# Performance work log

Measured on AMD Instinct MI355X. Metric: run time of the kernel, lower is better.

Reference implementation:

```python
import jax, jax.numpy as jnp
import numpy as np

N_EXPR, MAX_TOK, D = 8192, 32, 256
N_SYM, N_APP = 50000, 262144


def gate(prev, upd, Wg, bg, Wc, bc):
    # NDFA-style gated update: f*prev + (1-f)*candidate
    cat = jnp.concatenate([prev, upd], axis=-1)            # [N, 2D]
    f = jax.nn.sigmoid(cat @ Wg + bg)                      # [N, D]
    cand = jax.nn.relu(cat @ Wc + bc)                      # [N, D]
    return f * prev + (1.0 - f) * cand


def setup_inputs() -> dict:
    key = jax.random.key(0)
    ks = jax.random.split(key, 12)
    s = 1.0 / np.sqrt(2 * D)
    return {
        "expressions_encodings": jax.random.normal(ks[0], (N_EXPR, MAX_TOK, D), jnp.float32),
        "symbols_encodings": jax.random.normal(ks[1], (N_SYM, D), jnp.float32),
        "prev_cfg_nodes_encodings": jax.random.normal(ks[2], (N_EXPR, D), jnp.float32),
        "Wg1": jax.random.normal(ks[3], (2 * D, D), jnp.float32) * s,
        "bg1": jnp.zeros((D,), jnp.float32),
        "Wc1": jax.random.normal(ks[4], (2 * D, D), jnp.float32) * s,
        "bc1": jnp.zeros((D,), jnp.float32),
        "Wg2": jax.random.normal(ks[5], (2 * D, D), jnp.float32) * s,
        "bg2": jnp.zeros((D,), jnp.float32),
        "Wc2": jax.random.normal(ks[6], (2 * D, D), jnp.float32) * s,
        "bc2": jnp.zeros((D,), jnp.float32),
        "app_expr_idx": jax.random.randint(ks[7], (N_APP,), 0, N_EXPR, jnp.int32),
        "app_token_idx": jax.random.randint(ks[8], (N_APP,), 0, MAX_TOK, jnp.int32),
        "app_symbol_idx": jax.random.randint(ks[9], (N_APP,), 0, N_SYM, jnp.int32),
        "cfg_nodes_has_expression_mask": jnp.ones((N_EXPR,), jnp.bool_),
    }


def reference(expressions_encodings, symbols_encodings, prev_cfg_nodes_encodings,
              Wg1, bg1, Wc1, bc1, Wg2, bg2, Wc2, bc2,
              app_expr_idx, app_token_idx, app_symbol_idx,
              cfg_nodes_has_expression_mask):
    # --- AddSymbolsEncodingsToExpressions: gather -> gate -> scatter ---
    flat_idx = app_expr_idx * MAX_TOK + app_token_idx      # [N_APP]
    flat = expressions_encodings.reshape(-1, D)            # [N_EXPR*MAX_TOK, D]
    symbols_occurrences = flat[flat_idx]                   # gather [N_APP, D]
    sym_enc_for_occ = symbols_encodings[app_symbol_idx]    # gather [N_APP, D]
    updated_occ = gate(symbols_occurrences, sym_enc_for_occ, Wg1, bg1, Wc1, bc1)
    flat = flat.at[flat_idx].set(updated_occ)              # scatter (last-write like torch.scatter)
    updated_expressions = flat.reshape(N_EXPR, MAX_TOK, D)

    # --- combine tokens per expression (combiner proxy: mean over tokens) ---
    cfg_combined_expressions = updated_expressions.mean(axis=1)   # [N_EXPR, D]

    # --- CFGNodeEncodingMixerWithExpressionEncoding: gate + masked scatter ---
    gated_nodes = gate(prev_cfg_nodes_encodings, cfg_combined_expressions, Wg2, bg2, Wc2, bc2)
    new_nodes = jnp.where(cfg_nodes_has_expression_mask[:, None], gated_nodes,
                          prev_cfg_nodes_encodings)
    return new_nodes
```

## Files before the change

kernel.cpp:

```cpp
#include <hip/hip_runtime.h>
#include <hip/hip_bf16.h>

typedef __attribute__((ext_vector_type(8))) short bf16x8;
typedef __attribute__((ext_vector_type(4))) float f32x4;

#define NE 8192
#define MT 32
#define DD 256
#define NAPP 262144
#define NSLOT (NE*MT)
#define NSYM 50000
#define NSYMP 50048

#define WS_WINNER 0
#define WS_WTSW   (1u<<20)
#define WS_WTLIN  (2u<<20)
#define WS_SYMGC  (3u<<20)

static __device__ __forceinline__ unsigned short f2b(float x){
  union{float f; unsigned u;} v; v.f = x;
  unsigned r = (v.u + 0x7fffu + ((v.u>>16)&1u))>>16;
  return (unsigned short)r;
}
static __device__ __forceinline__ unsigned pk2(float a, float b){
  return (unsigned)f2b(a) | ((unsigned)f2b(b)<<16);
}
static __device__ __forceinline__ float bfl(unsigned w){ union{unsigned u; float f;} v; v.u = w<<16; return v.f; }
static __device__ __forceinline__ float bfh(unsigned w){ union{unsigned u; float f;} v; v.u = w & 0xffff0000u; return v.f; }
static __device__ __forceinline__ float frombf(unsigned short u){ union{unsigned x; float f;} v; v.x = ((unsigned)u)<<16; return v.f; }

static __device__ __forceinline__ void gload16(const void* g, void* l){
  __builtin_amdgcn_global_load_lds((const __attribute__((address_space(1))) void*)g,
                                   (__attribute__((address_space(3))) void*)l, 16, 0, 0);
}

__global__ void k_wt(const float* __restrict__ w0, const float* __restrict__ w1,
                     const float* __restrict__ w2, const float* __restrict__ w3,
                     char* __restrict__ wtsw, unsigned short* __restrict__ wtlin){
  int g = blockIdx.x*256 + threadIdx.x;
  int m = g >> 14;
  int kg = (g >> 8) & 63;
  int n = g & 255;
  const float* W = (m==0)?w0:(m==1)?w1:(m==2)?w2:w3;
  unsigned short v[8];
  #pragma unroll
  for (int i=0;i<8;i++) v[i] = f2b(W[(kg*8+i)*DD + n]);
  uint4 u;
  u.x = (unsigned)v[0] | ((unsigned)v[1]<<16);
  u.y = (unsigned)v[2] | ((unsigned)v[3]<<16);
  u.z = (unsigned)v[4] | ((unsigned)v[5]<<16);
  u.w = (unsigned)v[6] | ((unsigned)v[7]<<16);
  *(uint4*)(wtlin + (size_t)m*131072 + n*512 + kg*8) = u;
  int rot = ((kg & 3) + (n >> 1)) & 3;
  *(uint4*)(wtsw + (size_t)m*262144 + n*1024 + (kg>>2)*64 + rot*16) = u;
}

__global__ void k_winner(const int* __restrict__ ei, const int* __restrict__ ti,
                         int* __restrict__ winner){
  int i = blockIdx.x*256 + threadIdx.x;
  atomicMax(&winner[ei[i]*MT + ti[i]], i);
}

__global__ __launch_bounds__(512, 4)
void k_syms(const float* __restrict__ sym, const char* __restrict__ wtsw,
            unsigned short* __restrict__ symgc){
  __shared__ char Abuf[32768];
  __shared__ char Bbuf[32768];

  int tid = threadIdx.x, lane = tid & 63, wv = tid >> 6;
  int l15 = lane & 15, lg = lane >> 4;
  int wq = wv & 3; bool isC = wv >= 4;
  int s0 = blockIdx.x * 64;

  {
    int r = tid >> 3;
    int row = s0 + r;
    char* arow = Abuf + r*512;
    unsigned swz = (unsigned)((r & 15) << 4);
    if (row < NSYM){
      const float* src = sym + (size_t)row*DD;
      #pragma unroll
      for (int i=0;i<4;i++){
        int c = (tid & 7) + i*8;
        float4 x = *(const float4*)(src + c*8);
        float4 y = *(const float4*)(src + c*8 + 4);
        uint4 u; u.x=pk2(x.x,x.y); u.y=pk2(x.z,x.w); u.z=pk2(y.x,y.y); u.w=pk2(y.z,y.w);
        *(uint4*)(arow + ((c*16) ^ swz)) = u;
      }
    } else {
      uint4 u = {0,0,0,0};
      #pragma unroll
      for (int i=0;i<4;i++){
        int c = (tid & 7) + i*8;
        *(uint4*)(arow + ((c*16) ^ swz)) = u;
      }
    }
  }
  __syncthreads();

  f32x4 acc[4][4];
  f32x4 zz = {0.f,0.f,0.f,0.f};
  #pragma unroll
  for (int rt=0;rt<4;rt++)
    #pragma unroll
    for (int ct=0;ct<4;ct++) acc[rt][ct]=zz;

  const char* wbG = wtsw;
  const char* wbC = wtsw + 262144;

  for (int kt=0; kt<8; ++kt){
    __syncthreads();
    #pragma unroll
    for (int i=0;i<4;i++){
      int n = wv*64 + i*16 + (lane>>2);
      const char* src = ((n < 256)? wbG : wbC) + (size_t)(n & 255)*1024 + (8+kt)*64 + (lane&3)*16;
      gload16(src, Bbuf + n*64 + (lane&3)*16);
    }
    __syncthreads();
    int koff = kt*64 + lg*16;
    bf16x8 a[4], b[4];
    #pragma unroll
    for (int rt=0;rt<4;rt++)
      a[rt] = *(const bf16x8*)(Abuf + (rt*16 + l15)*512 + (koff ^ (l15<<4)));
    #pragma unroll
    for (int ct=0;ct<4;ct++){
      int nn = (isC?256:0) + wq*64 + ct*16 + l15;
      b[ct] = *(const bf16x8*)(Bbuf + nn*64 + (((lg + (nn>>1)) & 3)<<4));
    }
    #pragma unroll
    for (int rt=0;rt<4;rt++)
      #pragma unroll
      for (int ct=0;ct<4;ct++)
        acc[rt][ct] = __builtin_amdgcn_mfma_f32_16x16x32_bf16(a[rt], b[ct], acc[rt][ct], 0,0,0);
  }

  int cb = (isC?256:0) + wq*64;
  #pragma unroll
  for (int rt=0;rt<4;rt++)
    #pragma unroll
    for (int ct=0;ct<4;ct++)
      #pragma unroll
      for (int j=0;j<4;j++){
        int row = s0 + rt*16 + lg*4 + j;
        symgc[(size_t)row*512 + cb + ct*16 + l15] = f2b(acc[rt][ct][j]);
      }
}

__global__ __launch_bounds__(512, 4)
void k_gate1(const float* __restrict__ expr, const char* __restrict__ wtsw,
             const float* __restrict__ bg, const float* __restrict__ bc,
             const int* __restrict__ winner, const int* __restrict__ appsym,
             const unsigned short* __restrict__ symgc,
             float* __restrict__ outcomb){
  __shared__ char Abuf[32768];
  __shared__ char Bbuf[32768];

  int tid = threadIdx.x, lane = tid & 63, wv = tid >> 6;
  int l15 = lane & 15, lg = lane >> 4;
  int wq = wv & 3; bool isC = wv >= 4;
  int s0 = blockIdx.x * 64;

  int wn = winner[s0 + lane];
  int sidv = (wn >= 0) ? appsym[wn] : -1;

  {
    int r = tid >> 3;
    const float* src = expr + (size_t)(s0 + r)*DD;
    char* arow = Abuf + r*512;
    unsigned swz = (unsigned)((r & 15) << 4);
    #pragma unroll
    for (int i=0;i<4;i++){
      int c = (tid & 7) + i*8;
      float4 x = *(const float4*)(src + c*8);
      float4 y = *(const float4*)(src + c*8 + 4);
      uint4 u; u.x=pk2(x.x,x.y); u.y=pk2(x.z,x.w); u.z=pk2(y.x,y.y); u.w=pk2(y.z,y.w);
      *(uint4*)(arow + ((c*16) ^ swz)) = u;
    }
  }
  __syncthreads();

  f32x4 acc[4][4];
  f32x4 zz = {0.f,0.f,0.f,0.f};
  #pragma unroll
  for (int rt=0;rt<4;rt++)
    #pragma unroll
    for (int ct=0;ct<4;ct++) acc[rt][ct]=zz;

  const char* wbG = wtsw;
  const char* wbC = wtsw + 262144;

  for (int kt=0; kt<8; ++kt){
    __syncthreads();
    #pragma unroll
    for (int i=0;i<4;i++){
      int n = wv*64 + i*16 + (lane>>2);
      const char* src = ((n < 256)? wbG : wbC) + (size_t)(n & 255)*1024 + kt*64 + (lane&3)*16;
      gload16(src, Bbuf + n*64 + (lane&3)*16);
    }
    __syncthreads();
    int koff = kt*64 + lg*16;
    bf16x8 a[4], b[4];
    #pragma unroll
    for (int rt=0;rt<4;rt++)
      a[rt] = *(const bf16x8*)(Abuf + (rt*16 + l15)*512 + (koff ^ (l15<<4)));
    #pragma unroll
    for (int ct=0;ct<4;ct++){
      int nn = (isC?256:0) + wq*64 + ct*16 + l15;
      b[ct] = *(const bf16x8*)(Bbuf + nn*64 + (((lg + (nn>>1)) & 3)<<4));
    }
    #pragma unroll
    for (int rt=0;rt<4;rt++)
      #pragma unroll
      for (int ct=0;ct<4;ct++)
        acc[rt][ct] = __builtin_amdgcn_mfma_f32_16x16x32_bf16(a[rt], b[ct], acc[rt][ct], 0,0,0);
  }

  __syncthreads();
  char* fbuf = Abuf;
  char* cbuf = Bbuf;
  char* obuf = isC ? cbuf : fbuf;

  const float* bias = isC ? bc : bg;
  float bv[4];
  #pragma unroll
  for (int ct=0;ct<4;ct++) bv[ct] = bias[wq*64 + ct*16 + l15];

  #pragma unroll
  for (int rt=0;rt<4;rt++){
    int rowb = rt*16 + lg*4;
    int sid[4];
    #pragma unroll
    for (int j=0;j<4;j++){ int s = __shfl(sidv, rowb + j); sid[j] = (s < 0) ? 0 : s; }
    float sv[4][4];
    #pragma unroll
    for (int j=0;j<4;j++)
      #pragma unroll
      for (int ct=0;ct<4;ct++)
        sv[j][ct] = frombf(symgc[(size_t)sid[j]*512 + (isC?256:0) + wq*64 + ct*16 + l15]);
    #pragma unroll
    for (int ct=0;ct<4;ct++){
      float o[4];
      #pragma unroll
      for (int j=0;j<4;j++){
        float x = acc[rt][ct][j] + sv[j][ct] + bv[ct];
        o[j] = isC ? fmaxf(x, 0.f) : 1.f/(1.f + __expf(-x));
      }
      int col = wq*64 + ct*16 + l15;
      uint2 pw; pw.x = pk2(o[0], o[1]); pw.y = pk2(o[2], o[3]);
      *(uint2*)(obuf + ((col*128 + rowb*2) ^ ((col&15)<<3))) = pw;
    }
  }
  __syncthreads();

  {
    int eL = wv >> 2, q = wv & 3;
    int col = q*64 + lane;
    float ssum = 0.f;
    #pragma unroll
    for (int i=0;i<8;i++){
      unsigned xr = (unsigned)((col*128 + eL*64 + i*8) ^ ((col&15)<<3));
      uint2 fu = *(const uint2*)(fbuf + xr);
      uint2 cu = *(const uint2*)(cbuf + xr);
      float fvv[4] = { bfl(fu.x), bfh(fu.x), bfl(fu.y), bfh(fu.y) };
      float cvv[4] = { bfl(cu.x), bfh(cu.x), bfl(cu.y), bfh(cu.y) };
      #pragma unroll
      for (int j=0;j<4;j++){
        int row = eL*32 + i*4 + j;
        float pv = expr[(size_t)(s0 + row)*DD + col];
        int sact = __shfl(sidv, row);
        ssum += (sact >= 0) ? (fvv[j]*pv + (1.f - fvv[j])*cvv[j]) : pv;
      }
    }
    outcomb[(size_t)(blockIdx.x*2 + eL)*DD + col] = ssum * (1.f/32.f);
  }
}

__global__ __launch_bounds__(1024)
void k_gate2(const float* __restrict__ prevn, const float* comb,
             const float* __restrict__ bg, const float* __restrict__ bc,
             const unsigned short* __restrict__ Wgt, const unsigned short* __restrict__ Wct,
             float* out){
  __shared__ char A[64*1024];

  int tid  = threadIdx.x;
  int lane = tid & 63;
  int wv   = tid >> 6;
  int wr = wv >> 3, wc = wv & 7;
  int l15 = lane & 15, lg = lane >> 4;
  int e0 = blockIdx.x * 64;

  {
    int row = tid >> 4, cb = (tid & 15)*16;
    unsigned swz = (unsigned)((row&7)<<4);
    const float* src = prevn + (size_t)(e0+row)*DD + cb;
    const float* s2  = comb  + (size_t)(e0+row)*DD + cb;
    char* arow = A + row*1024;
    #pragma unroll
    for (int i=0;i<2;i++){
      float4 x = *(const float4*)(src + i*8);
      float4 y = *(const float4*)(src + i*8 + 4);
      uint4 u; u.x=pk2(x.x,x.y); u.y=pk2(x.z,x.w); u.z=pk2(y.x,y.y); u.w=pk2(y.z,y.w);
      *(uint4*)(arow + (((cb+i*8)*2) ^ swz)) = u;
    }
    #pragma unroll
    for (int i=0;i<2;i++){
      float4 x = *(const float4*)(s2 + i*8);
      float4 y = *(const float4*)(s2 + i*8 + 4);
      uint4 u; u.x=pk2(x.x,x.y); u.y=pk2(x.z,x.w); u.z=pk2(y.x,y.y); u.w=pk2(y.z,y.w);
      *(uint4*)(arow + (((256+cb+i*8)*2) ^ swz)) = u;
    }
  }
  __syncthreads();

  unsigned swzL = (unsigned)((l15&7)<<4);
  const char* pa0 = A + (wr*32 + l15)*1024;
  const char* pa1 = pa0 + 16*1024;
  const unsigned short* wg0 = Wgt + (size_t)(wc*32 + l15)*512 + lg*8;
  const unsigned short* wc0 = Wct + (size_t)(wc*32 + l15)*512 + lg*8;

  f32x4 accg[2][2], accc[2][2];
  f32x4 zz = {0.f,0.f,0.f,0.f};
  #pragma unroll
  for (int ri=0;ri<2;ri++){ accg[ri][0]=zz; accg[ri][1]=zz; accc[ri][0]=zz; accc[ri][1]=zz; }

  for (int ks=0; ks<16; ++ks){
    int koff = (ks*64 + lg*16) ^ (int)swzL;
    bf16x8 a0 = *(const bf16x8*)(pa0 + koff);
    bf16x8 a1 = *(const bf16x8*)(pa1 + koff);
    int kw = ks*32;
    #pragma unroll
    for (int ct=0; ct<2; ++ct){
      bf16x8 b = *(const bf16x8*)(wg0 + ct*16*512 + kw);
      accg[0][ct] = __builtin_amdgcn_mfma_f32_16x16x32_bf16(a0, b, accg[0][ct], 0,0,0);
      accg[1][ct] = __builtin_amdgcn_mfma_f32_16x16x32_bf16(a1, b, accg[1][ct], 0,0,0);
    }
  }

  float bgv[2], bcv[2];
  #pragma unroll
  for (int ct=0;ct<2;ct++){ int c = wc*32+ct*16+l15; bgv[ct]=bg[c]; bcv[ct]=bc[c]; }
  #pragma unroll
  for (int ri=0;ri<2;ri++)
    #pragma unroll
    for (int ct=0;ct<2;ct++)
      #pragma unroll
      for (int j=0;j<4;j++)
        accg[ri][ct][j] = 1.f/(1.f + __expf(-(accg[ri][ct][j] + bgv[ct])));

  for (int ks=0; ks<16; ++ks){
    int koff = (ks*64 + lg*16) ^ (int)swzL;
    bf16x8 a0 = *(const bf16x8*)(pa0 + koff);
    bf16x8 a1 = *(const bf16x8*)(pa1 + koff);
    int kw = ks*32;
    #pragma unroll
    for (int ct=0; ct<2; ++ct){
      bf16x8 b = *(const bf16x8*)(wc0 + ct*16*512 + kw);
      accc[0][ct] = __builtin_amdgcn_mfma_f32_16x16x32_bf16(a0, b, accc[0][ct], 0,0,0);
      accc[1][ct] = __builtin_amdgcn_mfma_f32_16x16x32_bf16(a1, b, accc[1][ct], 0,0,0);
    }
  }

  #pragma unroll
  for (int ct=0; ct<2; ++ct){
    #pragma unroll
    for (int ri=0; ri<2; ++ri){
      #pragma unroll
      for (int j=0;j<4;j++){
        int row = wr*32 + ri*16 + lg*4 + j;
        int col = wc*32 + ct*16 + l15;
        int e = e0 + row;
        float prevv = prevn[(size_t)e*DD + col];
        float fr = accg[ri][ct][j];
        float cand = fmaxf(accc[ri][ct][j] + bcv[ct], 0.f);
        out[(size_t)e*DD + col] = fr*prevv + (1.f-fr)*cand;
      }
    }
  }
}

extern "C" void kernel_launch(void* const* d_in, const int* in_sizes, int n_in,
                              void* d_out, int out_size, void* d_ws, size_t ws_size,
                              hipStream_t stream){
  const float* expr = (const float*)d_in[0];
  const float* sym  = (const float*)d_in[1];
  const float* prevn= (const float*)d_in[2];
  const float* Wg1 = (const float*)d_in[3];
  const float* bg1 = (const float*)d_in[4];
  const float* Wc1 = (const float*)d_in[5];
  const float* bc1 = (const float*)d_in[6];
  const float* Wg2 = (const float*)d_in[7];
  const float* bg2 = (const float*)d_in[8];
  const float* Wc2 = (const float*)d_in[9];
  const float* bc2 = (const float*)d_in[10];
  const int* aei = (const int*)d_in[11];
  const int* ati = (const int*)d_in[12];
  const int* asi = (const int*)d_in[13];
  float* outp = (float*)d_out;

  char* wsb = (char*)d_ws;
  int* winner = (int*)(wsb + WS_WINNER);
  char* wtsw = wsb + WS_WTSW;
  unsigned short* wtlin = (unsigned short*)(wsb + WS_WTLIN);
  unsigned short* symgc = (unsigned short*)(wsb + WS_SYMGC);

  hipMemsetAsync(winner, 0xFF, NSLOT*sizeof(int), stream);
  k_wt<<<256, 256, 0, stream>>>(Wg1, Wc1, Wg2, Wc2, wtsw, wtlin);
  k_winner<<<NAPP/256, 256, 0, stream>>>(aei, ati, winner);
  k_syms<<<NSYMP/64, 512, 0, stream>>>(sym, wtsw, symgc);
  k_gate1<<<NSLOT/64, 512, 0, stream>>>(expr, wtsw, bg1, bc1, winner, asi, symgc, outp);
  k_gate2<<<NE/64, 1024, 0, stream>>>(prevn, outp, bg2, bc2,
                                      wtlin + 262144, wtlin + 393216, outp);
}
```

Baseline: 278.3 us.

## Restructure gate1 so each wave computes gate and candidate columns with register epilogue

Each wave now owns 32 output columns for both the gate and candidate GEMMs, so the sigmoid/relu combine and the token-mean reduction run directly in registers through shuffles. This removes the bf16 round-trip through LDS and the extra barriers. The symbol projection table is re-laid out so gate and candidate values for a lane sit together and load as one ushort4. Weight staging is split into separate G and C buffers whose loads are interleaved with the MFMAs. Launch bounds drop to 2 blocks per CU to leave room for the larger per-thread accumulator sets, at some risk to occupancy.

```diff
diff --git a/kernel.cpp b/kernel.cpp
--- a/kernel.cpp
+++ b/kernel.cpp
@@ -25,8 +25,6 @@
 static __device__ __forceinline__ unsigned pk2(float a, float b){
   return (unsigned)f2b(a) | ((unsigned)f2b(b)<<16);
 }
-static __device__ __forceinline__ float bfl(unsigned w){ union{unsigned u; float f;} v; v.u = w<<16; return v.f; }
-static __device__ __forceinline__ float bfh(unsigned w){ union{unsigned u; float f;} v; v.u = w & 0xffff0000u; return v.f; }
 static __device__ __forceinline__ float frombf(unsigned short u){ union{unsigned x; float f;} v; v.x = ((unsigned)u)<<16; return v.f; }
 
 static __device__ __forceinline__ void gload16(const void* g, void* l){
@@ -134,7 +132,6 @@
         acc[rt][ct] = __builtin_amdgcn_mfma_f32_16x16x32_bf16(a[rt], b[ct], acc[rt][ct], 0,0,0);
   }
 
-  int cb = (isC?256:0) + wq*64;
   #pragma unroll
   for (int rt=0;rt<4;rt++)
     #pragma unroll
@@ -142,31 +139,36 @@
       #pragma unroll
       for (int j=0;j<4;j++){
         int row = s0 + rt*16 + lg*4 + j;
-        symgc[(size_t)row*512 + cb + ct*16 + l15] = f2b(acc[rt][ct][j]);
-      }
-}
-
-__global__ __launch_bounds__(512, 4)
+        int idx = (wq*2 + (ct>>1))*64 + l15*4 + (ct&1)*2 + (isC?1:0);
+        symgc[(size_t)row*512 + idx] = f2b(acc[rt][ct][j]);
+      }
+}
+
+__global__ __launch_bounds__(512, 2)
 void k_gate1(const float* __restrict__ expr, const char* __restrict__ wtsw,
              const float* __restrict__ bg, const float* __restrict__ bc,
              const int* __restrict__ winner, const int* __restrict__ appsym,
              const unsigned short* __restrict__ symgc,
              float* __restrict__ outcomb){
-  __shared__ char Abuf[32768];
-  __shared__ char Bbuf[32768];
+  __shared__ char A[32768];
+  __shared__ char BGb[16384];
+  __shared__ char BCb[16384];
 
   int tid = threadIdx.x, lane = tid & 63, wv = tid >> 6;
   int l15 = lane & 15, lg = lane >> 4;
-  int wq = wv & 3; bool isC = wv >= 4;
   int s0 = blockIdx.x * 64;
 
   int wn = winner[s0 + lane];
-  int sidv = (wn >= 0) ? appsym[wn] : -1;
+  int sidv = (wn >= 0) ? appsym[wn] : 0;
+  unsigned long long hwmask = __ballot(wn >= 0);
+
+  const char* wsG = wtsw;
+  const char* wsC = wtsw + 262144;
 
   {
     int r = tid >> 3;
     const float* src = expr + (size_t)(s0 + r)*DD;
-    char* arow = Abuf + r*512;
+    char* arow = A + r*512;
     unsigned swz = (unsigned)((r & 15) << 4);
     #pragma unroll
     for (int i=0;i<4;i++){
@@ -177,102 +179,108 @@
       *(uint4*)(arow + ((c*16) ^ swz)) = u;
     }
   }
+  {
+    #pragma unroll
+    for (int i=0;i<2;i++){
+      int g = tid + i*512;
+      int n = g >> 2, p = g & 3;
+      gload16(wsG + (size_t)n*1024 + p*16, BGb + g*16);
+      gload16(wsC + (size_t)n*1024 + p*16, BCb + g*16);
+    }
+  }
   __syncthreads();
 
-  f32x4 acc[4][4];
+  f32x4 accG[4][2], accC[4][2];
   f32x4 zz = {0.f,0.f,0.f,0.f};
   #pragma unroll
-  for (int rt=0;rt<4;rt++)
-    #pragma unroll
-    for (int ct=0;ct<4;ct++) acc[rt][ct]=zz;
-
-  const char* wbG = wtsw;
-  const char* wbC = wtsw + 262144;
+  for (int rt=0;rt<4;rt++){ accG[rt][0]=zz; accG[rt][1]=zz; accC[rt][0]=zz; accC[rt][1]=zz; }
+
+  int nl0 = wv*32 + l15;
+  int rot0 = ((lg + (nl0>>1)) & 3) << 4;
+  int rot1 = ((lg + ((nl0+16)>>1)) & 3) << 4;
+  int boff0 = nl0*64 + rot0;
+  int boff1 = (nl0+16)*64 + rot1;
 
   for (int kt=0; kt<8; ++kt){
+    if (kt > 0){
+      #pragma unroll
+      for (int i=0;i<2;i++){
+        int g = tid + i*512;
+        int n = g >> 2, p = g & 3;
+        gload16(wsC + (size_t)n*1024 + kt*64 + p*16, BCb + g*16);
+      }
+    }
+    int koff = kt*64 + lg*16;
+    bf16x8 a[4];
+    #pragma unroll
+    for (int rt=0;rt<4;rt++)
+      a[rt] = *(const bf16x8*)(A + (rt*16 + l15)*512 + (koff ^ (l15<<4)));
+    {
+      bf16x8 b0 = *(const bf16x8*)(BGb + boff0);
+      bf16x8 b1 = *(const bf16x8*)(BGb + boff1);
+      #pragma unroll
+      for (int rt=0;rt<4;rt++){
+        accG[rt][0] = __builtin_amdgcn_mfma_f32_16x16x32_bf16(a[rt], b0, accG[rt][0], 0,0,0);
+        accG[rt][1] = __builtin_amdgcn_mfma_f32_16x16x32_bf16(a[rt], b1, accG[rt][1], 0,0,0);
+      }
+    }
     __syncthreads();
-    #pragma unroll
-    for (int i=0;i<4;i++){
-      int n = wv*64 + i*16 + (lane>>2);
-      const char* src = ((n < 256)? wbG : wbC) + (size_t)(n & 255)*1024 + kt*64 + (lane&3)*16;
-      gload16(src, Bbuf + n*64 + (lane&3)*16);
+    if (kt < 7){
+      #pragma unroll
+      for (int i=0;i<2;i++){
+        int g = tid + i*512;
+        int n = g >> 2, p = g & 3;
+        gload16(wsG + (size_t)n*1024 + (kt+1)*64 + p*16, BGb + g*16);
+      }
+    }
+    {
+      bf16x8 b0 = *(const bf16x8*)(BCb + boff0);
+      bf16x8 b1 = *(const bf16x8*)(BCb + boff1);
+      #pragma unroll
+      for (int rt=0;rt<4;rt++){
+        accC[rt][0] = __builtin_amdgcn_mfma_f32_16x16x32_bf16(a[rt], b0, accC[rt][0], 0,0,0);
+        accC[rt][1] = __builtin_amdgcn_mfma_f32_16x16x32_bf16(a[rt], b1, accC[rt][1], 0,0,0);
+      }
     }
     __syncthreads();
-    int koff = kt*64 + lg*16;
-    bf16x8 a[4], b[4];
-    #pragma unroll
-    for (int rt=0;rt<4;rt++)
-      a[rt] = *(const bf16x8*)(Abuf + (rt*16 + l15)*512 + (koff ^ (l15<<4)));
-    #pragma unroll
-    for (int ct=0;ct<4;ct++){
-      int nn = (isC?256:0) + wq*64 + ct*16 + l15;
-      b[ct] = *(const bf16x8*)(Bbuf + nn*64 + (((lg + (nn>>1)) & 3)<<4));
-    }
-    #pragma unroll
-    for (int rt=0;rt<4;rt++)
-      #pragma unroll
-      for (int ct=0;ct<4;ct++)
-        acc[rt][ct] = __builtin_amdgcn_mfma_f32_16x16x32_bf16(a[rt], b[ct], acc[rt][ct], 0,0,0);
-  }
-
-  __syncthreads();
-  char* fbuf = Abuf;
-  char* cbuf = Bbuf;
-  char* obuf = isC ? cbuf : fbuf;
-
-  const float* bias = isC ? bc : bg;
-  float bv[4];
-  #pragma unroll
-  for (int ct=0;ct<4;ct++) bv[ct] = bias[wq*64 + ct*16 + l15];
-
+  }
+
+  float bgv[2], bcv[2];
+  #pragma unroll
+  for (int ct=0;ct<2;ct++){ int c = wv*32+ct*16+l15; bgv[ct]=bg[c]; bcv[ct]=bc[c]; }
+
+  float osum[2][2] = {{0.f,0.f},{0.f,0.f}};
   #pragma unroll
   for (int rt=0;rt<4;rt++){
-    int rowb = rt*16 + lg*4;
-    int sid[4];
-    #pragma unroll
-    for (int j=0;j<4;j++){ int s = __shfl(sidv, rowb + j); sid[j] = (s < 0) ? 0 : s; }
-    float sv[4][4];
-    #pragma unroll
-    for (int j=0;j<4;j++)
-      #pragma unroll
-      for (int ct=0;ct<4;ct++)
-        sv[j][ct] = frombf(symgc[(size_t)sid[j]*512 + (isC?256:0) + wq*64 + ct*16 + l15]);
-    #pragma unroll
-    for (int ct=0;ct<4;ct++){
-      float o[4];
-      #pragma unroll
-      for (int j=0;j<4;j++){
-        float x = acc[rt][ct][j] + sv[j][ct] + bv[ct];
-        o[j] = isC ? fmaxf(x, 0.f) : 1.f/(1.f + __expf(-x));
-      }
-      int col = wq*64 + ct*16 + l15;
-      uint2 pw; pw.x = pk2(o[0], o[1]); pw.y = pk2(o[2], o[3]);
-      *(uint2*)(obuf + ((col*128 + rowb*2) ^ ((col&15)<<3))) = pw;
-    }
-  }
-  __syncthreads();
-
-  {
-    int eL = wv >> 2, q = wv & 3;
-    int col = q*64 + lane;
-    float ssum = 0.f;
-    #pragma unroll
-    for (int i=0;i<8;i++){
-      unsigned xr = (unsigned)((col*128 + eL*64 + i*8) ^ ((col&15)<<3));
-      uint2 fu = *(const uint2*)(fbuf + xr);
-      uint2 cu = *(const uint2*)(cbuf + xr);
-      float fvv[4] = { bfl(fu.x), bfh(fu.x), bfl(fu.y), bfh(fu.y) };
-      float cvv[4] = { bfl(cu.x), bfh(cu.x), bfl(cu.y), bfh(cu.y) };
-      #pragma unroll
-      for (int j=0;j<4;j++){
-        int row = eL*32 + i*4 + j;
-        float pv = expr[(size_t)(s0 + row)*DD + col];
-        int sact = __shfl(sidv, row);
-        ssum += (sact >= 0) ? (fvv[j]*pv + (1.f - fvv[j])*cvv[j]) : pv;
-      }
-    }
-    outcomb[(size_t)(blockIdx.x*2 + eL)*DD + col] = ssum * (1.f/32.f);
-  }
+    #pragma unroll
+    for (int j=0;j<4;j++){
+      int row = rt*16 + lg*4 + j;
+      int sid = __shfl(sidv, row);
+      const ushort4 sv = *(const ushort4*)(symgc + (size_t)sid*512 + wv*64 + l15*4);
+      bool hw = (hwmask >> row) & 1ull;
+      const float* prow = expr + (size_t)(s0+row)*DD;
+      #pragma unroll
+      for (int ct=0;ct<2;ct++){
+        float p = prow[wv*32 + ct*16 + l15];
+        float gl = accG[rt][ct][j] + frombf(sv[ct*2+0]) + bgv[ct];
+        float cl = accC[rt][ct][j] + frombf(sv[ct*2+1]) + bcv[ct];
+        float f = 1.f/(1.f + __expf(-gl));
+        float cd = fmaxf(cl, 0.f);
+        float o = hw ? (f*p + (1.f-f)*cd) : p;
+        osum[rt>>1][ct] += o;
+      }
+    }
+  }
+  #pragma unroll
+  for (int e=0;e<2;e++)
+    #pragma unroll
+    for (int ct=0;ct<2;ct++){
+      float s = osum[e][ct];
+      s += __shfl_xor(s, 16);
+      s += __shfl_xor(s, 32);
+      if (lane < 16)
+        outcomb[(size_t)(blockIdx.x*2 + e)*DD + wv*32 + ct*16 + l15] = s * (1.f/32.f);
+    }
 }
 
 __global__ __launch_bounds__(1024)
```

New measurement: 318.0 us. 1.14x slower.
